# Performance work log

Measured on AMD Instinct MI355X. Metric: run time of the kernel, lower is better.

Reference implementation:

```python
import jax, jax.numpy as jnp
import numpy as np

# ---- config (from init_kwargs) ----
XBOUND = (-51.2, 51.2, 0.8)
YBOUND = (-51.2, 51.2, 0.8)
ZBOUND = (-3.0, 1.0, 0.5)
FINAL_DIM = (512, 512)   # (H, W) of raw images
XV, YV, ZV = 128, 128, 8  # voxel grid dims from bounds
EPS = 1e-6


def setup_inputs() -> dict:
    key = jax.random.key(0)
    kf, ki, ke = jax.random.split(key, 3)
    feats = jax.random.normal(kf, (2, 4, 64, 64, 64), jnp.float32)   # B,N,C,Hf,Wf (post-CamEncode)
    intrins = jax.random.normal(ki, (2, 4, 4, 4), jnp.float32)       # B,N,4,4 pix_T_cam
    extrins = jax.random.normal(ke, (2, 4, 4, 4), jnp.float32)       # B,N,4,4 cam0_T_camX
    return {"feats": feats, "intrins": intrins, "extrins": extrins}


def _safe_inverse(a):
    # rigid-transform inverse: R^T, -R^T t; last row copied through (geom.safe_inverse)
    rT = jnp.swapaxes(a[:, :3, :3], 1, 2)
    t = -jnp.einsum('bij,bj->bi', rT, a[:, :3, 3])
    top = jnp.concatenate([rT, t[:, :, None]], axis=2)
    return jnp.concatenate([top, a[:, 3:4, :]], axis=1)


def _scale_intrinsics(K, sx, sy):
    # geom.scale_intrinsics: rebuild clean 4x4 intrinsics with scaled fx,fy,x0,y0
    BN = K.shape[0]
    Kn = jnp.zeros((BN, 4, 4), K.dtype)
    Kn = Kn.at[:, 0, 0].set(K[:, 0, 0] * sx)
    Kn = Kn.at[:, 1, 1].set(K[:, 1, 1] * sy)
    Kn = Kn.at[:, 0, 2].set(K[:, 0, 2] * sx)
    Kn = Kn.at[:, 1, 2].set(K[:, 1, 2] * sy)
    Kn = Kn.at[:, 2, 2].set(1.0)
    Kn = Kn.at[:, 3, 3].set(1.0)
    return Kn


def _grid_sample_zeros(feat, x, y):
    # F.grid_sample(..., align_corners=False, padding='zeros') at pixel coords (x,y)
    # feat: (BN,C,H,W); x,y: (BN,P)
    BN, C, H, W = feat.shape
    px = x - 0.5  # unnormalized sample position (align_corners=False)
    py = y - 0.5
    x0f = jnp.floor(px); y0f = jnp.floor(py)
    wx = px - x0f; wy = py - y0f
    x0 = x0f.astype(jnp.int32); y0 = y0f.astype(jnp.int32)
    featf = feat.reshape(BN, C, H * W)

    def corner(xi, yi, w):
        valid = (xi >= 0) & (xi < W) & (yi >= 0) & (yi < H)
        idx = jnp.clip(yi, 0, H - 1) * W + jnp.clip(xi, 0, W - 1)
        g = jnp.take_along_axis(featf, idx[:, None, :], axis=2)  # (BN,C,P)
        return g * (w * valid.astype(w.dtype))[:, None, :]

    return (corner(x0, y0, (1 - wx) * (1 - wy)) + corner(x0 + 1, y0, wx * (1 - wy))
            + corner(x0, y0 + 1, (1 - wx) * wy) + corner(x0 + 1, y0 + 1, wx * wy))


def _mem_grid_cam0():
    # gridcloud3d (Z,Y,X order) mapped Mem->Ref: ref = mem*vox + MIN + vox/2
    vsx = (XBOUND[1] - XBOUND[0]) / XV
    vsy = (YBOUND[1] - YBOUND[0]) / YV
    vsz = (ZBOUND[1] - ZBOUND[0]) / ZV
    gz, gy, gx = jnp.meshgrid(jnp.arange(ZV, dtype=jnp.float32),
                              jnp.arange(YV, dtype=jnp.float32),
                              jnp.arange(XV, dtype=jnp.float32), indexing='ij')
    xc = gx * vsx + (XBOUND[0] + vsx / 2)
    yc = gy * vsy + (YBOUND[0] + vsy / 2)
    zc = gz * vsz + (ZBOUND[0] + vsz / 2)
    return jnp.stack([xc, yc, zc], axis=-1).reshape(ZV * YV * XV, 3)  # (P,3)


def reference(feats, intrins, extrins):
    B, N, C, Hf, Wf = feats.shape
    BN = B * N
    feats_ = feats.reshape(BN, C, Hf, Wf)
    K = intrins.reshape(BN, 4, 4)
    E = extrins.reshape(BN, 4, 4)

    camX_T_cam0 = _safe_inverse(E)
    sy = Hf / float(FINAL_DIM[0])
    sx = Wf / float(FINAL_DIM[1])
    featpix_T_cam = _scale_intrinsics(K, sx, sy)
    pix_T_cam0 = jnp.einsum('bij,bjk->bik', featpix_T_cam, camX_T_cam0)

    xyz_cam0 = _mem_grid_cam0()  # (P,3)

    def apply44(T, p):  # (BN,4,4) x (P,3) -> (BN,P,3)
        return jnp.einsum('bij,pj->bpi', T[:, :3, :3], p) + T[:, None, :3, 3]

    xyz_camX = apply44(camX_T_cam0, xyz_cam0)
    z = xyz_camX[..., 2]
    xyz_pix = apply44(pix_T_cam0, xyz_cam0)
    denom = jnp.maximum(xyz_pix[..., 2:3], EPS)  # clamp(min=EPS)
    x = xyz_pix[..., 0] / denom[..., 0]
    y = xyz_pix[..., 1] / denom[..., 0]

    valid = ((x > -0.5) & (x < float(Wf) - 0.5) & (y > -0.5) & (y < float(Hf) - 0.5)
             & (z > 0.0)).astype(feats.dtype)  # (BN,P)

    vals = _grid_sample_zeros(feats_, x, y) * valid[:, None, :]  # (BN,C,P)
    feat_mems = vals.reshape(B, N, C, ZV, YV, XV)

    mask = (jnp.abs(feat_mems) > 0).astype(feats.dtype)
    feat_mem = jnp.sum(feat_mems * mask, axis=1) / (EPS + jnp.sum(mask, axis=1))  # (B,C,Z,Y,X)

    feat_mem = jnp.transpose(feat_mem, (0, 1, 4, 3, 2))      # b c X Y Z (permute 0,1,4,3,2)
    out = jnp.transpose(feat_mem, (0, 1, 4, 2, 3)).reshape(B, C * ZV, XV, YV)  # b (c z) h w
    return out
```

## Files before the change

### kernel.cpp

```cpp
#include <hip/hip_runtime.h>
#include <hip/hip_fp16.h>

#define BB     2
#define NN     4
#define CC     64
#define HF     64
#define WF     64
#define XVOX   128
#define YVOX   128
#define ZVOX   8
#define BN_TOT (BB * NN)
#define FEATS_PER_BN (CC * HF * WF)
#define OUT_C_STRIDE (ZVOX * XVOX * YVOX)
#define OUT_B_STRIDE (CC * OUT_C_STRIDE)

__global__ __launch_bounds__(256) void transpose_feats_kernel(
    const float* __restrict__ in, __half* __restrict__ outT) {
    __shared__ float tile[64 * 65];
    int bh = blockIdx.x;
    int bn = bh >> 6;
    int h  = bh & 63;
    int t  = threadIdx.x;

    const float* src = in + bn * FEATS_PER_BN + h * WF;
#pragma unroll
    for (int k = 0; k < 16; ++k) {
        int idx = t + k * 256;
        int c = idx >> 6;
        int w = idx & 63;
        tile[w * 65 + c] = src[c * (HF * WF) + w];
    }
    __syncthreads();
    __half* dst = outT + bn * FEATS_PER_BN + h * (WF * CC);
#pragma unroll
    for (int k = 0; k < 8; ++k) {
        int idx = t + k * 256;
        int w  = idx >> 5;
        int c2 = idx & 31;
        float a = tile[w * 65 + 2 * c2];
        float b = tile[w * 65 + 2 * c2 + 1];
        *reinterpret_cast<__half2*>(dst + w * CC + 2 * c2) =
            __halves2half2(__float2half(a), __float2half(b));
    }
}

__device__ inline float4 ld_half4(const __half* __restrict__ p) {
    uint2 u = *reinterpret_cast<const uint2*>(p);
    float2 f0 = __half22float2(*reinterpret_cast<const __half2*>(&u.x));
    float2 f1 = __half22float2(*reinterpret_cast<const __half2*>(&u.y));
    return make_float4(f0.x, f0.y, f1.x, f1.y);
}

__global__ __launch_bounds__(256) void bev_splat_kernel(
    const __half* __restrict__ featsT,
    const float* __restrict__ intrins,
    const float* __restrict__ extrins,
    float* __restrict__ out) {
    __shared__ float mats_s[NN * 12];
    __shared__ __align__(16) int   offs_s[64][NN][4];
    __shared__ __align__(16) float wgts_s[64][NN][4];
    __shared__ float tile[64 * 65];

    int lg   = blockIdx.x;
    int half = lg & 1;
    int vx   = (lg >> 1) & 127;
    int vz   = (lg >> 8) & 7;
    int b    = lg >> 11;
    int vy0  = half * 64;

    if (threadIdx.x < NN) {
        int n  = threadIdx.x;
        int bn = b * NN + n;
        const float* e = extrins + bn * 16;
        const float* k = intrins + bn * 16;
        float inv[3][4];
#pragma unroll
        for (int i = 0; i < 3; ++i) {
            inv[i][0] = e[0 * 4 + i];
            inv[i][1] = e[1 * 4 + i];
            inv[i][2] = e[2 * 4 + i];
            inv[i][3] = -(e[0 * 4 + i] * e[0 * 4 + 3] +
                          e[1 * 4 + i] * e[1 * 4 + 3] +
                          e[2 * 4 + i] * e[2 * 4 + 3]);
        }
        float fx = k[0] * 0.125f;
        float fy = k[5] * 0.125f;
        float cx = k[2] * 0.125f;
        float cy = k[6] * 0.125f;
        float* m = mats_s + n * 12;
#pragma unroll
        for (int j = 0; j < 4; ++j) {
            m[j]     = fx * inv[0][j] + cx * inv[2][j];
            m[4 + j] = fy * inv[1][j] + cy * inv[2][j];
            m[8 + j] = inv[2][j];
        }
    }
    __syncthreads();

    bool validFlag;
    {
        int v  = threadIdx.x >> 2;
        int n  = threadIdx.x & 3;
        int vy = vy0 + v;
        float xc = vx * 0.8f - 50.8f;
        float yc = vy * 0.8f - 50.8f;
        float zc = vz * 0.5f - 2.75f;
        const float* M = mats_s + n * 12;
        float px = M[0] * xc + M[1] * yc + M[2]  * zc + M[3];
        float py = M[4] * xc + M[5] * yc + M[6]  * zc + M[7];
        float pz = M[8] * xc + M[9] * yc + M[10] * zc + M[11];
        float denom = fmaxf(pz, 1e-6f);
        float sx = px / denom;
        float sy = py / denom;
        bool valid = (sx > -0.5f) && (sx < (float)WF - 0.5f) &&
                     (sy > -0.5f) && (sy < (float)HF - 0.5f) && (pz > 0.0f);
        validFlag = valid;
        int base = (b * NN + n) * FEATS_PER_BN;
        int   o[4];
        float w[4];
        if (valid) {
            float gx = sx - 0.5f;
            float gy = sy - 0.5f;
            float x0f = floorf(gx), y0f = floorf(gy);
            float wx = gx - x0f,    wy = gy - y0f;
            int x0 = (int)x0f, y0 = (int)y0f;
            int   xs[2]  = {x0, x0 + 1};
            int   ys[2]  = {y0, y0 + 1};
            float wxs[2] = {1.0f - wx, wx};
            float wys[2] = {1.0f - wy, wy};
#pragma unroll
            for (int ky = 0; ky < 2; ++ky) {
#pragma unroll
                for (int kx = 0; kx < 2; ++kx) {
                    int kk = ky * 2 + kx;
                    int xi = xs[kx], yi = ys[ky];
                    bool cv = (xi >= 0) && (xi < WF) && (yi >= 0) && (yi < HF);
                    int xic = min(max(xi, 0), WF - 1);
                    int yic = min(max(yi, 0), HF - 1);
                    o[kk] = base + (yic * WF + xic) * CC;
                    w[kk] = cv ? (wxs[kx] * wys[ky]) : 0.0f;
                }
            }
        } else {
#pragma unroll
            for (int kk = 0; kk < 4; ++kk) { o[kk] = base; w[kk] = 0.0f; }
        }
#pragma unroll
        for (int kk = 0; kk < 4; ++kk) {
            offs_s[v][n][kk] = o[kk];
            wgts_s[v][n][kk] = w[kk];
        }
    }

    int nvalid = __syncthreads_count(validFlag ? 1 : 0);

    int obase = b * OUT_B_STRIDE + vz * (XVOX * YVOX) + vx * YVOX + vy0;

    if (nvalid == 0) {
        float4 z = make_float4(0.f, 0.f, 0.f, 0.f);
#pragma unroll
        for (int it = 0; it < 4; ++it) {
            int l4 = threadIdx.x + it * 256;
            int c  = l4 >> 4;
            int v  = (l4 & 15) << 2;
            *reinterpret_cast<float4*>(out + obase + c * OUT_C_STRIDE + v) = z;
        }
        return;
    }

    int wave = threadIdx.x >> 6;
    int lane = threadIdx.x & 63;
    int l16  = lane & 15;
    int vsub = lane >> 4;
    const __half* fT = featsT + (l16 << 2);

#pragma unroll
    for (int g = 0; g < 4; ++g) {
        int v = wave * 16 + g * 4 + vsub;
        float n0 = 0.f, n1 = 0.f, n2 = 0.f, n3 = 0.f;
        float c0 = 0.f, c1 = 0.f, c2 = 0.f, c3 = 0.f;
#pragma unroll
        for (int n = 0; n < NN; ++n) {
            int4   o = *reinterpret_cast<const int4*>(&offs_s[v][n][0]);
            float4 w = *reinterpret_cast<const float4*>(&wgts_s[v][n][0]);
            float wsum = (w.x + w.y) + (w.z + w.w);
            if (wsum != 0.0f) {
                float4 ga = ld_half4(fT + o.x);
                float4 gb = ld_half4(fT + o.y);
                float4 gc = ld_half4(fT + o.z);
                float4 gd = ld_half4(fT + o.w);
                float v0 = w.x * ga.x; v0 += w.y * gb.x; v0 += w.z * gc.x; v0 += w.w * gd.x;
                float v1 = w.x * ga.y; v1 += w.y * gb.y; v1 += w.z * gc.y; v1 += w.w * gd.y;
                float v2 = w.x * ga.z; v2 += w.y * gb.z; v2 += w.z * gc.z; v2 += w.w * gd.z;
                float v3 = w.x * ga.w; v3 += w.y * gb.w; v3 += w.z * gc.w; v3 += w.w * gd.w;
                n0 += v0; n1 += v1; n2 += v2; n3 += v3;
                c0 += (v0 != 0.0f) ? 1.0f : 0.0f;
                c1 += (v1 != 0.0f) ? 1.0f : 0.0f;
                c2 += (v2 != 0.0f) ? 1.0f : 0.0f;
                c3 += (v3 != 0.0f) ? 1.0f : 0.0f;
            }
        }
        float* tr = tile + v * 65 + (l16 << 2);
        tr[0] = n0 / (1e-6f + c0);
        tr[1] = n1 / (1e-6f + c1);
        tr[2] = n2 / (1e-6f + c2);
        tr[3] = n3 / (1e-6f + c3);
    }
    __syncthreads();

#pragma unroll
    for (int it = 0; it < 4; ++it) {
        int l4 = threadIdx.x + it * 256;
        int c  = l4 >> 4;
        int v  = (l4 & 15) << 2;
        float4 r;
        r.x = tile[(v + 0) * 65 + c];
        r.y = tile[(v + 1) * 65 + c];
        r.z = tile[(v + 2) * 65 + c];
        r.w = tile[(v + 3) * 65 + c];
        *reinterpret_cast<float4*>(out + obase + c * OUT_C_STRIDE + v) = r;
    }
}

extern "C" void kernel_launch(void* const* d_in, const int* in_sizes, int n_in,
                              void* d_out, int out_size, void* d_ws, size_t ws_size,
                              hipStream_t stream) {
    const float* feats   = (const float*)d_in[0];
    const float* intrins = (const float*)d_in[1];
    const float* extrins = (const float*)d_in[2];
    float* out = (float*)d_out;

    __half* featsT = (__half*)d_ws;

    transpose_feats_kernel<<<BN_TOT * HF, 256, 0, stream>>>(feats, featsT);

    int nblk = BB * ZVOX * XVOX * 2;
    bev_splat_kernel<<<nblk, 256, 0, stream>>>(featsT, intrins, extrins, out);
}
```

Measured before the change: 101.7 us.

## Widen gathers to 8 halves per lane, swizzle block order, replace division

```diff
diff --git a/kernel.cpp b/kernel.cpp
--- a/kernel.cpp
+++ b/kernel.cpp
@@ -13,6 +13,7 @@
 #define FEATS_PER_BN (CC * HF * WF)
 #define OUT_C_STRIDE (ZVOX * XVOX * YVOX)
 #define OUT_B_STRIDE (CC * OUT_C_STRIDE)
+#define TS 68
 
 __global__ __launch_bounds__(256) void transpose_feats_kernel(
     const float* __restrict__ in, __half* __restrict__ outT) {
@@ -44,11 +45,14 @@
     }
 }
 
-__device__ inline float4 ld_half4(const __half* __restrict__ p) {
-    uint2 u = *reinterpret_cast<const uint2*>(p);
-    float2 f0 = __half22float2(*reinterpret_cast<const __half2*>(&u.x));
-    float2 f1 = __half22float2(*reinterpret_cast<const __half2*>(&u.y));
-    return make_float4(f0.x, f0.y, f1.x, f1.y);
+__device__ inline void ld_half8(const __half* __restrict__ p, float f[8]) {
+    uint4 u = *reinterpret_cast<const uint4*>(p);
+    float2 a = __half22float2(*reinterpret_cast<const __half2*>(&u.x));
+    float2 b = __half22float2(*reinterpret_cast<const __half2*>(&u.y));
+    float2 c = __half22float2(*reinterpret_cast<const __half2*>(&u.z));
+    float2 d = __half22float2(*reinterpret_cast<const __half2*>(&u.w));
+    f[0] = a.x; f[1] = a.y; f[2] = b.x; f[3] = b.y;
+    f[4] = c.x; f[5] = c.y; f[6] = d.x; f[7] = d.y;
 }
 
 __global__ __launch_bounds__(256) void bev_splat_kernel(
@@ -59,9 +63,11 @@
     __shared__ float mats_s[NN * 12];
     __shared__ __align__(16) int   offs_s[64][NN][4];
     __shared__ __align__(16) float wgts_s[64][NN][4];
-    __shared__ float tile[64 * 65];
-
-    int lg   = blockIdx.x;
+    __shared__ __align__(16) float tile[64 * TS];
+
+    int blk = blockIdx.x;
+    int lg  = ((blk & 7) << 9) | (blk >> 3);
+
     int half = lg & 1;
     int vx   = (lg >> 1) & 127;
     int vz   = (lg >> 8) & 7;
@@ -170,41 +176,53 @@
 
     int wave = threadIdx.x >> 6;
     int lane = threadIdx.x & 63;
-    int l16  = lane & 15;
-    int vsub = lane >> 4;
-    const __half* fT = featsT + (l16 << 2);
-
-#pragma unroll
-    for (int g = 0; g < 4; ++g) {
-        int v = wave * 16 + g * 4 + vsub;
-        float n0 = 0.f, n1 = 0.f, n2 = 0.f, n3 = 0.f;
-        float c0 = 0.f, c1 = 0.f, c2 = 0.f, c3 = 0.f;
+    int l8   = lane & 7;
+    int vsub = lane >> 3;
+    const __half* fT = featsT + (l8 << 3);
+
+    const float RC0 = 1.0f / (1e-6f);
+    const float RC1 = 1.0f / (1e-6f + 1.0f);
+    const float RC2 = 1.0f / (1e-6f + 2.0f);
+    const float RC3 = 1.0f / (1e-6f + 3.0f);
+    const float RC4 = 1.0f / (1e-6f + 4.0f);
+
+#pragma unroll
+    for (int g = 0; g < 2; ++g) {
+        int v = wave * 16 + g * 8 + vsub;
+        float acc[8]  = {0.f, 0.f, 0.f, 0.f, 0.f, 0.f, 0.f, 0.f};
+        float cntf[8] = {0.f, 0.f, 0.f, 0.f, 0.f, 0.f, 0.f, 0.f};
 #pragma unroll
         for (int n = 0; n < NN; ++n) {
             int4   o = *reinterpret_cast<const int4*>(&offs_s[v][n][0]);
             float4 w = *reinterpret_cast<const float4*>(&wgts_s[v][n][0]);
             float wsum = (w.x + w.y) + (w.z + w.w);
             if (wsum != 0.0f) {
-                float4 ga = ld_half4(fT + o.x);
-                float4 gb = ld_half4(fT + o.y);
-                float4 gc = ld_half4(fT + o.z);
-                float4 gd = ld_half4(fT + o.w);
-                float v0 = w.x * ga.x; v0 += w.y * gb.x; v0 += w.z * gc.x; v0 += w.w * gd.x;
-                float v1 = w.x * ga.y; v1 += w.y * gb.y; v1 += w.z * gc.y; v1 += w.w * gd.y;
-                float v2 = w.x * ga.z; v2 += w.y * gb.z; v2 += w.z * gc.z; v2 += w.w * gd.z;
-                float v3 = w.x * ga.w; v3 += w.y * gb.w; v3 += w.z * gc.w; v3 += w.w * gd.w;
-                n0 += v0; n1 += v1; n2 += v2; n3 += v3;
-                c0 += (v0 != 0.0f) ? 1.0f : 0.0f;
-                c1 += (v1 != 0.0f) ? 1.0f : 0.0f;
-                c2 += (v2 != 0.0f) ? 1.0f : 0.0f;
-                c3 += (v3 != 0.0f) ? 1.0f : 0.0f;
+                float ga[8], gb[8], gc[8], gd[8];
+                ld_half8(fT + o.x, ga);
+                ld_half8(fT + o.y, gb);
+                ld_half8(fT + o.z, gc);
+                ld_half8(fT + o.w, gd);
+#pragma unroll
+                for (int j = 0; j < 8; ++j) {
+                    float vj = w.x * ga[j];
+                    vj += w.y * gb[j];
+                    vj += w.z * gc[j];
+                    vj += w.w * gd[j];
+                    acc[j]  += vj;
+                    cntf[j] += (vj != 0.0f) ? 1.0f : 0.0f;
+                }
             }
         }
-        float* tr = tile + v * 65 + (l16 << 2);
-        tr[0] = n0 / (1e-6f + c0);
-        tr[1] = n1 / (1e-6f + c1);
-        tr[2] = n2 / (1e-6f + c2);
-        tr[3] = n3 / (1e-6f + c3);
+        float* tr = tile + v * TS + (l8 << 3);
+#pragma unroll
+        for (int j = 0; j < 8; ++j) {
+            float cj = cntf[j];
+            float inv = (cj <= 0.5f) ? RC0 :
+                        (cj <= 1.5f) ? RC1 :
+                        (cj <= 2.5f) ? RC2 :
+                        (cj <= 3.5f) ? RC3 : RC4;
+            tr[j] = acc[j] * inv;
+        }
     }
     __syncthreads();
 
@@ -214,10 +232,10 @@
         int c  = l4 >> 4;
         int v  = (l4 & 15) << 2;
         float4 r;
-        r.x = tile[(v + 0) * 65 + c];
-        r.y = tile[(v + 1) * 65 + c];
-        r.z = tile[(v + 2) * 65 + c];
-        r.w = tile[(v + 3) * 65 + c];
+        r.x = tile[(v + 0) * TS + c];
+        r.y = tile[(v + 1) * TS + c];
+        r.z = tile[(v + 2) * TS + c];
+        r.w = tile[(v + 3) * TS + c];
         *reinterpret_cast<float4*>(out + obase + c * OUT_C_STRIDE + v) = r;
     }
 }
```

Result: no change. 101.9 us (+0.2%).
